# Kernel tuning notes

Measured on AMD Instinct MI355X. Metric: run time of the kernel, lower is better.

Reference implementation:

```python
import jax, jax.numpy as jnp
import numpy as np

NX, NY = 4096, 4096


def setup_inputs() -> dict:
    key = jax.random.key(0)
    k1, k2 = jax.random.split(key)
    u_main = jax.random.normal(k1, (NX, NY), dtype=jnp.float32)
    u_coupled = jax.random.normal(k2, (NX, NY), dtype=jnp.float32)
    D_eff = jnp.array([0.05], dtype=jnp.float32)
    dirichlet_val = jnp.array([1.0, 0.0, 1.0, 0.0], dtype=jnp.float32)
    stencil = jnp.array([1.0, -1.0], dtype=jnp.float32)  # fixed [1,-1] stencil
    return {
        "u_main": u_main,
        "u_coupled": u_coupled,
        "D_eff": D_eff,
        "dirichlet_val": dirichlet_val,
        "stencil": stencil,
        "t": 1,
    }


def reference(u_main, u_coupled, D_eff, dirichlet_val, stencil, t):
    # Flux_Kernels.forward with Dirichlet BCs on all four boundaries and
    # is_retardation_a_func=False (ret_inv = ones), so u_coupled and t are unused.
    D = D_eff[0]
    s0, s1 = stencil[0], stencil[1]
    ret = jnp.ones_like(u_main)  # ret_inv when no retardation function

    # left (x- direction): boundary row 0, neighbors rows 1..Nx-1
    left_bound = ((s0 * dirichlet_val[0] + s1 * u_main[0, :]) * D * ret[0, :])[None, :]
    left_nb = (s0 * u_main[:-1, :] + s1 * u_main[1:, :]) * D * ret[1:, :]
    left_flux = jnp.concatenate([left_bound, left_nb], axis=0)

    # right (x+ direction): neighbors rows 0..Nx-2, boundary row Nx-1
    right_bound = ((s0 * dirichlet_val[1] + s1 * u_main[-1, :]) * D * ret[-1, :])[None, :]
    right_nb = (s0 * u_main[1:, :] + s1 * u_main[:-1, :]) * D * ret[:-1, :]
    right_flux = jnp.concatenate([right_nb, right_bound], axis=0)

    # top (y- direction): boundary col 0, neighbors cols 1..Ny-1
    top_bound = ((s0 * dirichlet_val[2] + s1 * u_main[:, 0]) * D * ret[:, 0])[:, None]
    top_nb = (s0 * u_main[:, :-1] + s1 * u_main[:, 1:]) * D * ret[:, 1:]
    top_flux = jnp.concatenate([top_bound, top_nb], axis=1)

    # bottom (y+ direction): neighbors cols 0..Ny-2, boundary col Ny-1
    bottom_bound = ((s0 * dirichlet_val[3] + s1 * u_main[:, -1]) * D * ret[:, -1])[:, None]
    bottom_nb = (s0 * u_main[:, 1:] + s1 * u_main[:, :-1]) * D * ret[:, :-1]
    bottom_flux = jnp.concatenate([bottom_nb, bottom_bound], axis=1)

    return left_flux + right_flux + top_flux + bottom_flux
```

## Files before the change

kernel.cpp:

```cpp
#include <hip/hip_runtime.h>
#include <cstdint>


#define NX 4096
#define NY 4096
#define TR 32
#define TC 256
#define HR (TR + 2)
#define LSTRIDE 264
#define COL_L 260
#define COL_R 261

typedef float float4v __attribute__((ext_vector_type(4)));

__device__ __forceinline__ void row_to_lds(const float* gsrc_lane, float* lds_row_base) {
    __builtin_amdgcn_global_load_lds(
        (const __attribute__((address_space(1))) uint32_t*)gsrc_lane,
        (__attribute__((address_space(3))) uint32_t*)lds_row_base,
        16, 0, 0);
}

__global__ __launch_bounds__(256, 4) void flux_stencil_kernel(
    const float* __restrict__ u,
    const float* __restrict__ D_eff,
    const float* __restrict__ dv,
    const float* __restrict__ st,
    float* __restrict__ out)
{
    __shared__ float s[HR * LSTRIDE];

    const float D  = D_eff[0];
    const float s0 = st[0];
    const float s1 = st[1];
    const float k1 = D * s0;
    const float k4 = 4.0f * D * s1;
    const float dvUp = dv[0], dvDn = dv[1], dvL = dv[2], dvR = dv[3];

    const int b    = blockIdx.x;
    const int X    = b & 7;
    const int r    = b >> 3;
    const int ct   = r & 15;
    const int band = X * 16 + (r >> 4);
    const int i0   = band * TR;
    const int j0   = ct * TC;

    const int t    = threadIdx.x;
    const int w    = t >> 6;
    const int lane = t & 63;

    const bool topEdge = (i0 == 0);
    const bool botEdge = (i0 + TR == NX);

    for (int k = w; k < HR; k += 4) {
        int gr = i0 + k - 1;
        gr = gr < 0 ? 0 : (gr > NX - 1 ? NX - 1 : gr);
        row_to_lds(u + (size_t)gr * NY + j0 + 4 * lane, &s[k * LSTRIDE]);
    }

    if (t < TR) {
        const int k  = 1 + t;
        const int gr = i0 + k - 1;
        s[k * LSTRIDE + COL_L] = (j0 == 0) ? dvL : u[(size_t)gr * NY + j0 - 1];
    } else if (t >= 64 && t < 64 + TR) {
        const int k  = 1 + (t - 64);
        const int gr = i0 + k - 1;
        s[k * LSTRIDE + COL_R] = (j0 + TC == NY) ? dvR : u[(size_t)gr * NY + j0 + TC];
    }

    __syncthreads();

    #pragma unroll
    for (int rr = 0; rr < 8; ++rr) {
        const int k = 1 + w * 8 + rr;
        const float* rowc = &s[k * LSTRIDE];

        float4v up = *(const float4v*)&s[(k - 1) * LSTRIDE + 4 * lane];
        float4v c  = *(const float4v*)&rowc[4 * lane];
        float4v dn = *(const float4v*)&s[(k + 1) * LSTRIDE + 4 * lane];

        const float lft = rowc[lane == 0  ? COL_L : 4 * lane - 1];
        const float rgt = rowc[lane == 63 ? COL_R : 4 * lane + 4];

        if (topEdge && k == 1)  { up.x = dvUp; up.y = dvUp; up.z = dvUp; up.w = dvUp; }
        if (botEdge && k == TR) { dn.x = dvDn; dn.y = dvDn; dn.z = dvDn; dn.w = dvDn; }

        float4v o;
        o.x = k1 * (up.x + dn.x + lft + c.y) + k4 * c.x;
        o.y = k1 * (up.y + dn.y + c.x + c.z) + k4 * c.y;
        o.z = k1 * (up.z + dn.z + c.y + c.w) + k4 * c.z;
        o.w = k1 * (up.w + dn.w + c.z + rgt) + k4 * c.w;

        *(float4v*)(out + (size_t)(i0 + k - 1) * NY + j0 + 4 * lane) = o;
    }
}

extern "C" void kernel_launch(void* const* d_in, const int* in_sizes, int n_in,
                              void* d_out, int out_size, void* d_ws, size_t ws_size,
                              hipStream_t stream) {
    const float* u_main    = (const float*)d_in[0];
    const float* D_eff     = (const float*)d_in[2];
    const float* dirichlet = (const float*)d_in[3];
    const float* stencil   = (const float*)d_in[4];
    float* outp = (float*)d_out;

    const int grid  = 2048;
    const int block = 256;

    flux_stencil_kernel<<<grid, block, 0, stream>>>(u_main, D_eff, dirichlet, stencil, outp);
}
```

Measured before the change: 24.50 us.

## Double-buffer LDS row chunks with async loads across four chunks per block

Each block now processes four 32-row chunks with two LDS buffers, issuing async global-to-LDS loads for the next chunk while computing the current one, using explicit vmcnt waits and barriers. Halo columns are also loaded asynchronously into LDS, and the grid shrinks to 512 blocks with lower occupancy bounds. This aims to hide load latency and amortize launch and setup cost per block, but it relies on hand-counted vmcnt values and has fewer blocks in flight for latency hiding.

```diff
diff --git a/kernel.cpp b/kernel.cpp
--- a/kernel.cpp
+++ b/kernel.cpp
@@ -5,29 +5,40 @@
 #define NX 4096
 #define NY 4096
 #define TR 32
+#define HR (TR + 2)
 #define TC 256
-#define HR (TR + 2)
 #define LSTRIDE 264
-#define COL_L 260
-#define COL_R 261
+#define HOFF (HR * LSTRIDE)
+#define BUF_FLOATS (HOFF + 128)
+#define CHUNKS 4
 
 typedef float float4v __attribute__((ext_vector_type(4)));
 
-__device__ __forceinline__ void row_to_lds(const float* gsrc_lane, float* lds_row_base) {
+__device__ __forceinline__ void row_to_lds(const float* g, float* l) {
     __builtin_amdgcn_global_load_lds(
-        (const __attribute__((address_space(1))) uint32_t*)gsrc_lane,
-        (__attribute__((address_space(3))) uint32_t*)lds_row_base,
-        16, 0, 0);
+        (const __attribute__((address_space(1))) uint32_t*)g,
+        (__attribute__((address_space(3))) uint32_t*)l, 16, 0, 0);
+}
+__device__ __forceinline__ void sc_to_lds(const float* g, float* l) {
+    __builtin_amdgcn_global_load_lds(
+        (const __attribute__((address_space(1))) uint32_t*)g,
+        (__attribute__((address_space(3))) uint32_t*)l, 4, 0, 0);
 }
 
-__global__ __launch_bounds__(256, 4) void flux_stencil_kernel(
+#define WAIT_VM(NSTR) { asm volatile("s_waitcnt vmcnt(" NSTR ")" ::: "memory"); \
+                        __builtin_amdgcn_sched_barrier(0); }
+#define WAIT_LGKM0    { asm volatile("s_waitcnt lgkmcnt(0)" ::: "memory");      \
+                        __builtin_amdgcn_sched_barrier(0); }
+#define BAR           __builtin_amdgcn_s_barrier();
+
+__global__ __launch_bounds__(256, 2) void flux_stencil_kernel(
     const float* __restrict__ u,
     const float* __restrict__ D_eff,
     const float* __restrict__ dv,
     const float* __restrict__ st,
     float* __restrict__ out)
 {
-    __shared__ float s[HR * LSTRIDE];
+    __shared__ float s[2][BUF_FLOATS];
 
     const float D  = D_eff[0];
     const float s0 = st[0];
@@ -40,58 +51,89 @@
     const int X    = b & 7;
     const int r    = b >> 3;
     const int ct   = r & 15;
-    const int band = X * 16 + (r >> 4);
-    const int i0   = band * TR;
+    const int band = X * 4 + (r >> 4);
     const int j0   = ct * TC;
+    const int i0b  = band * (TR * CHUNKS);
 
     const int t    = threadIdx.x;
     const int w    = t >> 6;
     const int lane = t & 63;
 
-    const bool topEdge = (i0 == 0);
-    const bool botEdge = (i0 + TR == NX);
+    const bool lEdgeCol = (j0 == 0);
+    const bool rEdgeCol = (j0 + TC == NY);
 
-    for (int k = w; k < HR; k += 4) {
-        int gr = i0 + k - 1;
-        gr = gr < 0 ? 0 : (gr > NX - 1 ? NX - 1 : gr);
-        row_to_lds(u + (size_t)gr * NY + j0 + 4 * lane, &s[k * LSTRIDE]);
+    #define STAGE(m)                                                           \
+    {                                                                          \
+        float* sb = s[(m) & 1];                                                \
+        const int i0 = i0b + (m) * TR;                                         \
+        for (int k = w; k < HR; k += 4) {                    \
+            int gr = i0 + k - 1;                                               \
+            gr = gr < 0 ? 0 : (gr > NX - 1 ? NX - 1 : gr);                     \
+            row_to_lds(u + (size_t)gr * NY + j0 + 4 * lane, sb + k * LSTRIDE); \
+        }                                                                      \
+        if (w == 2) {                                       \
+            const int gr  = i0 + (lane < TR ? lane : TR - 1);                  \
+            const int col = lEdgeCol ? 0 : j0 - 1;                             \
+            sc_to_lds(u + (size_t)gr * NY + col, sb + HOFF);                   \
+        }                                                                      \
+        if (w == 3) {                                      \
+            const int gr  = i0 + (lane < TR ? lane : TR - 1);                  \
+            const int col = rEdgeCol ? NY - 1 : j0 + TC;                       \
+            sc_to_lds(u + (size_t)gr * NY + col, sb + HOFF + 64);              \
+        }                                                                      \
     }
 
-    if (t < TR) {
-        const int k  = 1 + t;
-        const int gr = i0 + k - 1;
-        s[k * LSTRIDE + COL_L] = (j0 == 0) ? dvL : u[(size_t)gr * NY + j0 - 1];
-    } else if (t >= 64 && t < 64 + TR) {
-        const int k  = 1 + (t - 64);
-        const int gr = i0 + k - 1;
-        s[k * LSTRIDE + COL_R] = (j0 + TC == NY) ? dvR : u[(size_t)gr * NY + j0 + TC];
+    #define COMPUTE(m)                                                         \
+    {                                                                          \
+        const float* sb = s[(m) & 1];                                          \
+        const int i0 = i0b + (m) * TR;                                         \
+        const bool topE = (band == 0)  && ((m) == 0);                          \
+        const bool botE = (band == 31) && ((m) == CHUNKS - 1);                 \
+        const int cOff = 4 * lane;                                             \
+        const int lOff = (lane == 0) ? 0 : cOff - 4;                           \
+        const int rOff = cOff + 4;                  \
+        _Pragma("unroll")                                                      \
+        for (int rr8 = 0; rr8 < 8; ++rr8) {                                    \
+            const int rr = w * 8 + rr8;               \
+            const int k  = rr + 1;                                             \
+            const float* rowc = sb + k * LSTRIDE;                              \
+            float4v up = *(const float4v*)(sb + (k - 1) * LSTRIDE + cOff);     \
+            float4v c  = *(const float4v*)(rowc + cOff);                       \
+            float4v dn = *(const float4v*)(sb + (k + 1) * LSTRIDE + cOff);     \
+            const float4v lv = *(const float4v*)(rowc + lOff);                 \
+            const float4v rv = *(const float4v*)(rowc + rOff);                 \
+            const float hl = sb[HOFF + rr];                \
+            const float hr = sb[HOFF + 64 + rr];                               \
+            const float lft = (lane == 0)  ? (lEdgeCol ? dvL : hl) : lv.w;     \
+            const float rgt = (lane == 63) ? (rEdgeCol ? dvR : hr) : rv.x;     \
+            if (topE && rr == 0)      { up.x=dvUp; up.y=dvUp; up.z=dvUp; up.w=dvUp; } \
+            if (botE && rr == TR - 1) { dn.x=dvDn; dn.y=dvDn; dn.z=dvDn; dn.w=dvDn; } \
+            float4v o;                                                         \
+            o.x = k1 * (up.x + dn.x + lft + c.y) + k4 * c.x;                   \
+            o.y = k1 * (up.y + dn.y + c.x + c.z) + k4 * c.y;                   \
+            o.z = k1 * (up.z + dn.z + c.y + c.w) + k4 * c.z;                   \
+            o.w = k1 * (up.w + dn.w + c.z + rgt) + k4 * c.w;                   \
+            *(float4v*)(out + (size_t)(i0 + rr) * NY + j0 + cOff) = o;         \
+        }                                                                      \
     }
 
-    __syncthreads();
+    STAGE(0)
+    STAGE(1)
+    WAIT_VM("9")  BAR
+    COMPUTE(0)
+    WAIT_LGKM0    BAR
+    STAGE(2)
+    WAIT_VM("17") BAR
+    COMPUTE(1)
+    WAIT_LGKM0    BAR
+    STAGE(3)
+    WAIT_VM("17") BAR
+    COMPUTE(2)
+    WAIT_VM("8")  BAR
+    COMPUTE(3)
 
-    #pragma unroll
-    for (int rr = 0; rr < 8; ++rr) {
-        const int k = 1 + w * 8 + rr;
-        const float* rowc = &s[k * LSTRIDE];
-
-        float4v up = *(const float4v*)&s[(k - 1) * LSTRIDE + 4 * lane];
-        float4v c  = *(const float4v*)&rowc[4 * lane];
-        float4v dn = *(const float4v*)&s[(k + 1) * LSTRIDE + 4 * lane];
-
-        const float lft = rowc[lane == 0  ? COL_L : 4 * lane - 1];
-        const float rgt = rowc[lane == 63 ? COL_R : 4 * lane + 4];
-
-        if (topEdge && k == 1)  { up.x = dvUp; up.y = dvUp; up.z = dvUp; up.w = dvUp; }
-        if (botEdge && k == TR) { dn.x = dvDn; dn.y = dvDn; dn.z = dvDn; dn.w = dvDn; }
-
-        float4v o;
-        o.x = k1 * (up.x + dn.x + lft + c.y) + k4 * c.x;
-        o.y = k1 * (up.y + dn.y + c.x + c.z) + k4 * c.y;
-        o.z = k1 * (up.z + dn.z + c.y + c.w) + k4 * c.z;
-        o.w = k1 * (up.w + dn.w + c.z + rgt) + k4 * c.w;
-
-        *(float4v*)(out + (size_t)(i0 + k - 1) * NY + j0 + 4 * lane) = o;
-    }
+    #undef STAGE
+    #undef COMPUTE
 }
 
 extern "C" void kernel_launch(void* const* d_in, const int* in_sizes, int n_in,
@@ -103,7 +145,7 @@
     const float* stencil   = (const float*)d_in[4];
     float* outp = (float*)d_out;
 
-    const int grid  = 2048;
+    const int grid  = 512;
     const int block = 256;
 
     flux_stencil_kernel<<<grid, block, 0, stream>>>(u_main, D_eff, dirichlet, stencil, outp);
```

Result: slower. 26.55 us (+8.4%).
